# Optimization experiments

Hardware: AMD Instinct MI355X
Metric: run time of the kernel (lower is better)

## Reference

```python
import jax, jax.numpy as jnp
import numpy as np
import math

B, T, E, H = 2, 2048, 1024, 16
HD = E // H


def layernorm(x, g, b, eps=1e-5):
    mu = jnp.mean(x, axis=-1, keepdims=True)
    var = jnp.var(x, axis=-1, keepdims=True)
    return (x - mu) * jax.lax.rsqrt(var + eps) * g + b


def new_gelu(x):
    c = math.sqrt(2.0 / math.pi)
    return 0.5 * x * (1.0 + jnp.tanh(c * (x + 0.044715 * x ** 3)))


def setup_inputs() -> dict:
    key = jax.random.key(0)
    ks = jax.random.split(key, 6)
    s = 0.02
    return {
        "x": jax.random.normal(ks[0], (B, T, E), jnp.float32),
        "ln1_g": jnp.ones((E,), jnp.float32),
        "ln1_b": jnp.zeros((E,), jnp.float32),
        "w_attn": jax.random.normal(ks[1], (E, 3 * E), jnp.float32) * s,
        "b_attn": jnp.zeros((3 * E,), jnp.float32),
        "w_proj": jax.random.normal(ks[2], (E, E), jnp.float32) * s,
        "b_proj": jnp.zeros((E,), jnp.float32),
        "ln2_g": jnp.ones((E,), jnp.float32),
        "ln2_b": jnp.zeros((E,), jnp.float32),
        "w_fc": jax.random.normal(ks[3], (E, 4 * E), jnp.float32) * s,
        "b_fc": jnp.zeros((4 * E,), jnp.float32),
        "w_fc2": jax.random.normal(ks[4], (4 * E, E), jnp.float32) * s,
        "b_fc2": jnp.zeros((E,), jnp.float32),
    }


def reference(x, ln1_g, ln1_b, w_attn, b_attn, w_proj, b_proj,
              ln2_g, ln2_b, w_fc, b_fc, w_fc2, b_fc2):
    # --- attention branch (pre-norm) ---
    h = layernorm(x, ln1_g, ln1_b)
    qkv = h @ w_attn + b_attn                      # [B,T,3E]
    q, k, v = jnp.split(qkv, 3, axis=-1)
    # [B,T,E] -> [B,H,T,HD]
    q = q.reshape(B, T, H, HD).transpose(0, 2, 1, 3)
    k = k.reshape(B, T, H, HD).transpose(0, 2, 1, 3)
    v = v.reshape(B, T, H, HD).transpose(0, 2, 1, 3)
    att = jnp.einsum('bhqd,bhkd->bhqk', q, k) * (1.0 / math.sqrt(HD))
    causal = jnp.tril(jnp.ones((T, T), bool))       # [T,T]
    att = jnp.where(causal, att, -jnp.inf)
    att = jax.nn.softmax(att, axis=-1)
    y = jnp.einsum('bhqk,bhkd->bhqd', att, v)       # [B,H,T,HD]
    y = y.transpose(0, 2, 1, 3).reshape(B, T, E)
    y = y @ w_proj + b_proj
    x = x + y
    # --- MLP branch (pre-norm) ---
    h = layernorm(x, ln2_g, ln2_b)
    h = new_gelu(h @ w_fc + b_fc)
    h = h @ w_fc2 + b_fc2
    return x + h
```

## Files before the change

kernel.cpp:

```cpp
#include <hip/hip_runtime.h>

typedef unsigned short u16;
typedef unsigned int   u32;
typedef short bf16x8 __attribute__((ext_vector_type(8)));
typedef float f32x4  __attribute__((ext_vector_type(4)));

__device__ __forceinline__ float bf_lo(u32 u){ return __uint_as_float(u << 16); }
__device__ __forceinline__ float bf_hi(u32 u){ return __uint_as_float(u & 0xffff0000u); }
__device__ __forceinline__ u16 bf16r(float f){
  u32 u = __float_as_uint(f);
  u += 0x7fffu + ((u >> 16) & 1u);
  return (u16)(u >> 16);
}
__device__ __forceinline__ u32 pack2(float a, float b){
  return (u32)bf16r(a) | ((u32)bf16r(b) << 16);
}
__device__ __forceinline__ u32 pk_trunc(float a, float b){
  return (__float_as_uint(a) >> 16) | (__float_as_uint(b) & 0xffff0000u);
}
__device__ __forceinline__ float gelu_f(float x){
  float t = 0.7978845608028654f * (x + 0.044715f * x * x * x);
  t = fminf(fmaxf(t, -12.f), 12.f);
  float e = __expf(2.f * t);
  float th = (e - 1.f) / (e + 1.f);
  return 0.5f * x * (1.f + th);
}
__device__ __forceinline__ void glds16(const void* g, void* l) {
  __builtin_amdgcn_global_load_lds(
      (const __attribute__((address_space(1))) void*)g,
      (__attribute__((address_space(3))) void*)l, 16, 0, 0);
}

#define QSCALE 0.1803368801111204f

__device__ __forceinline__ void wt_body(const float* __restrict__ W,
                                        u16* __restrict__ Wt, int K, int N,
                                        int kx, int nx) {
  __shared__ float t[32][33];
  int k0 = kx * 32, n0 = nx * 32;
  int tx = threadIdx.x & 31, ty = threadIdx.x >> 5;
  #pragma unroll
  for (int i = 0; i < 32; i += 8)
    t[ty + i][tx] = W[(size_t)(k0 + ty + i) * N + n0 + tx];
  __syncthreads();
  #pragma unroll
  for (int i = 0; i < 32; i += 8)
    Wt[(size_t)(n0 + ty + i) * K + k0 + tx] = bf16r(t[tx][ty + i]);
}

__device__ __forceinline__ void ln_body(const float* __restrict__ x,
                                        const float* __restrict__ g,
                                        const float* __restrict__ bta,
                                        u16* __restrict__ out, int row) {
  int tid = threadIdx.x;
  const float4 xv = ((const float4*)(x + (size_t)row * 1024))[tid];
  float s = xv.x + xv.y + xv.z + xv.w;
  float q = xv.x*xv.x + xv.y*xv.y + xv.z*xv.z + xv.w*xv.w;
  #pragma unroll
  for (int off = 32; off > 0; off >>= 1) {
    s += __shfl_down(s, off);
    q += __shfl_down(q, off);
  }
  __shared__ float ss[4], sq[4];
  if ((tid & 63) == 0) { ss[tid >> 6] = s; sq[tid >> 6] = q; }
  __syncthreads();
  s = ss[0] + ss[1] + ss[2] + ss[3];
  q = sq[0] + sq[1] + sq[2] + sq[3];
  float mu = s * (1.f/1024.f);
  float rs = rsqrtf(q * (1.f/1024.f) - mu*mu + 1e-5f);
  const float4 gv = ((const float4*)g)[tid];
  const float4 bv = ((const float4*)bta)[tid];
  uint2 o;
  o.x = pack2((xv.x-mu)*rs*gv.x + bv.x, (xv.y-mu)*rs*gv.y + bv.y);
  o.y = pack2((xv.z-mu)*rs*gv.z + bv.z, (xv.w-mu)*rs*gv.w + bv.w);
  ((uint2*)(out + (size_t)row * 1024))[tid] = o;
}

__global__ __launch_bounds__(256) void prep_k(
    const float* __restrict__ w_attn, const float* __restrict__ w_proj,
    const float* __restrict__ w_fc,   const float* __restrict__ w_fc2,
    u16* __restrict__ wt_attn, u16* __restrict__ wt_proj,
    u16* __restrict__ wt_fc,   u16* __restrict__ wt_fc2,
    const float* __restrict__ x, const float* __restrict__ g,
    const float* __restrict__ b, u16* __restrict__ h1)
{
  int i = blockIdx.x;
  if (i < 3072)       wt_body(w_attn, wt_attn, 1024, 3072, i & 31, i >> 5);
  else if (i < 4096)  { int j = i - 3072; wt_body(w_proj, wt_proj, 1024, 1024, j & 31, j >> 5); }
  else if (i < 8192)  { int j = i - 4096; wt_body(w_fc,   wt_fc,   1024, 4096, j & 31, j >> 5); }
  else if (i < 12288) { int j = i - 8192; wt_body(w_fc2,  wt_fc2,  4096, 1024, j & 127, j >> 7); }
  else                ln_body(x, g, b, h1, i - 12288);
}

__global__ __launch_bounds__(256) void vt_k(const u16* __restrict__ qkv,
                                            u16* __restrict__ Vt) {
  __shared__ u16 tl[32][33];
  int t0 = blockIdx.x * 32;
  int bh = blockIdx.y >> 1, d0 = (blockIdx.y & 1) * 32;
  int bb = bh >> 4, h = bh & 15;
  int tx = threadIdx.x & 31, ty = threadIdx.x >> 5;
  #pragma unroll
  for (int i = 0; i < 32; i += 8)
    tl[ty + i][tx] = qkv[(size_t)(bb*2048 + t0 + ty + i)*3072 + 2048 + h*64 + d0 + tx];
  __syncthreads();
  #pragma unroll
  for (int i = 0; i < 32; i += 8)
    Vt[((size_t)bh*64 + d0 + ty + i)*2048 + t0 + tx] = tl[tx][ty + i];
}

__global__ __launch_bounds__(256) void ln_k(const float* __restrict__ x,
                                            const float* __restrict__ g,
                                            const float* __restrict__ bta,
                                            u16* __restrict__ out) {
  ln_body(x, g, bta, out, blockIdx.x);
}

template<int MODE, int MI, int LB>
__global__ __launch_bounds__(256, LB) void gemm_k(
    const u16* __restrict__ A, const u16* __restrict__ Bt,
    const float* __restrict__ bias, const float* __restrict__ resid,
    void* __restrict__ out, int M, int N, int K, int lda)
{
  constexpr int TM = MI * 32;
  __shared__ u16 Al[TM * 64];
  __shared__ u16 Bl[128 * 64];
  const int tid = threadIdx.x;
  const int by = blockIdx.y;
  const int sp = (MODE == 5) ? (by >> 3) : 0;
  const int n0 = (MODE == 5) ? ((by & 7) * 128) : (by * 128);
  const size_t koff = (size_t)sp * K;
  const int m0 = blockIdx.x * TM;
  const int wave = tid >> 6, lane = tid & 63;
  const int wm = (wave >> 1) * (MI * 16), wn = (wave & 1) * 64;
  const int l15 = lane & 15, quad = lane >> 4;
  const int sr = lane >> 3, cs = lane & 7;
  f32x4 acc[MI][4];
  const f32x4 zero = {0.f, 0.f, 0.f, 0.f};
  #pragma unroll
  for (int i = 0; i < MI; ++i)
    #pragma unroll
    for (int j = 0; j < 4; ++j)
      acc[i][j] = zero;
  for (int k0 = 0; k0 < K; k0 += 64) {
    __syncthreads();
    #pragma unroll
    for (int it = 0; it < MI; ++it) {
      int r = it*32 + wave*8 + sr;
      int c = cs ^ (r & 7);
      glds16(&A[(size_t)(m0 + r) * lda + koff + k0 + c*8], &Al[(it*32 + wave*8) * 64]);
    }
    #pragma unroll
    for (int it = 0; it < 4; ++it) {
      int r = it*32 + wave*8 + sr;
      int c = cs ^ (r & 7);
      glds16(&Bt[(size_t)(n0 + r) * lda + koff + k0 + c*8], &Bl[(it*32 + wave*8) * 64]);
    }
    __syncthreads();
    #pragma unroll
    for (int kk = 0; kk < 2; ++kk) {
      bf16x8 af[MI], bfr[4];
      #pragma unroll
      for (int i = 0; i < MI; ++i) {
        int R = wm + i*16 + l15;
        af[i] = *(const bf16x8*)&Al[R*64 + ((kk*4 + quad) ^ (R & 7)) * 8];
      }
      #pragma unroll
      for (int j = 0; j < 4; ++j) {
        int R = wn + j*16 + l15;
        bfr[j] = *(const bf16x8*)&Bl[R*64 + ((kk*4 + quad) ^ (R & 7)) * 8];
      }
      #pragma unroll
      for (int i = 0; i < MI; ++i)
        #pragma unroll
        for (int j = 0; j < 4; ++j)
          acc[i][j] = __builtin_amdgcn_mfma_f32_16x16x32_bf16(af[i], bfr[j], acc[i][j], 0, 0, 0);
    }
  }
  #pragma unroll
  for (int i = 0; i < MI; ++i) {
    #pragma unroll
    for (int j = 0; j < 4; ++j) {
      int col = n0 + wn + j*16 + l15;
      float bv = (MODE == 5) ? 0.f : bias[col];
      float sc = (MODE == 4 && col < 1024) ? QSCALE : 1.0f;
      #pragma unroll
      for (int r = 0; r < 4; ++r) {
        int row = m0 + wm + i*16 + quad*4 + r;
        size_t idx = (size_t)row * N + col;
        float v = acc[i][j][r] + bv;
        if constexpr (MODE == 0)      ((u16*)out)[idx] = bf16r(v);
        else if constexpr (MODE == 1) ((float*)out)[idx] = v + resid[idx];
        else if constexpr (MODE == 2) ((u16*)out)[idx] = bf16r(gelu_f(v));
        else if constexpr (MODE == 4) ((u16*)out)[idx] = bf16r(v * sc);
        else if constexpr (MODE == 5) ((u16*)out)[(size_t)sp*M*N + idx] = bf16r(v);
        else                          ((float*)out)[idx] = v + resid[idx];
      }
    }
  }
}

__global__ __launch_bounds__(256) void cmb_k(const u16* __restrict__ p,
                                             const float* __restrict__ bias,
                                             const float* __restrict__ x2,
                                             float* __restrict__ out) {
  int row = blockIdx.x, t = threadIdx.x;
  size_t i = (size_t)row * 1024 + t*4;
  uint2 a = *(const uint2*)&p[i];
  uint2 b = *(const uint2*)&p[4194304 + i];
  float4 xv = ((const float4*)x2)[i >> 2];
  float4 bv = ((const float4*)bias)[t];
  float4 o;
  o.x = bf_lo(a.x) + bf_lo(b.x) + bv.x + xv.x;
  o.y = bf_hi(a.x) + bf_hi(b.x) + bv.y + xv.y;
  o.z = bf_lo(a.y) + bf_lo(b.y) + bv.z + xv.z;
  o.w = bf_hi(a.y) + bf_hi(b.y) + bv.w + xv.w;
  ((float4*)out)[i >> 2] = o;
}

__global__ __launch_bounds__(256, 4) void attn_k(const u16* __restrict__ qkv,
                                                 const u16* __restrict__ Vt,
                                                 u16* __restrict__ y) {
  __shared__ u16 Kl[64*64];
  __shared__ u16 Vl[64*64];
  __shared__ u16 Pw[4*16*72];
  const int tid = threadIdx.x;
  const int bh = blockIdx.x & 31, bb = bh >> 4, h = bh & 15;
  const int qt = 31 - (int)(blockIdx.x >> 5);
  const int w = tid >> 6, lane = tid & 63;
  const int l15 = lane & 15, quad = lane >> 4;
  const int sr = lane >> 3, cs = lane & 7;
  u16* Pme = Pw + w * (16*72);
  const int w16l = w*16 + l15;
  const int dquad = quad*4;

  const u16* qp = qkv + ((size_t)(bb*2048 + qt*64 + w16l))*3072 + h*64 + quad*8;
  const bf16x8 aq0 = *(const bf16x8*)qp;
  const bf16x8 aq1 = *(const bf16x8*)(qp + 32);

  f32x4 o[4];
  const f32x4 zero = {0.f,0.f,0.f,0.f};
  #pragma unroll
  for (int dt = 0; dt < 4; ++dt) o[dt] = zero;
  float l = 0.f;

  const u16* kbase = qkv + (size_t)bb*2048*3072 + 1024 + h*64;
  const u16* vbase = Vt + (size_t)bh*64*2048;

  for (int kt = 0; kt <= qt; ++kt) {
    __syncthreads();
    #pragma unroll
    for (int it = 0; it < 2; ++it) {
      int r = it*32 + w*8 + sr;
      int c = cs ^ (r & 7);
      glds16(kbase + (size_t)(kt*64 + r)*3072 + c*8, &Kl[(it*32 + w*8) * 64]);
      glds16(vbase + (size_t)r*2048 + kt*64 + c*8,   &Vl[(it*32 + w*8) * 64]);
    }
    __syncthreads();
    bf16x8 ak[4][2], av[4][2];
    #pragma unroll
    for (int nt = 0; nt < 4; ++nt) {
      int R = nt*16 + l15;
      #pragma unroll
      for (int kk = 0; kk < 2; ++kk) {
        ak[nt][kk] = *(const bf16x8*)&Kl[R*64 + ((kk*4 + quad) ^ (R & 7)) * 8];
        av[nt][kk] = *(const bf16x8*)&Vl[R*64 + ((kk*4 + quad) ^ (R & 7)) * 8];
      }
    }
    f32x4 sv[4];
    #pragma unroll
    for (int nt = 0; nt < 4; ++nt) {
      f32x4 s = zero;
      s = __builtin_amdgcn_mfma_f32_16x16x32_bf16(ak[nt][0], aq0, s, 0, 0, 0);
      s = __builtin_amdgcn_mfma_f32_16x16x32_bf16(ak[nt][1], aq1, s, 0, 0, 0);
      sv[nt] = s;
    }
    if (kt == qt) {
      #pragma unroll
      for (int nt = 0; nt < 4; ++nt)
        #pragma unroll
        for (int r = 0; r < 4; ++r)
          if (nt*16 + dquad + r > w16l) sv[nt][r] = -1e30f;
    }
    float pv[4][4];
    #pragma unroll
    for (int nt = 0; nt < 4; ++nt)
      #pragma unroll
      for (int r = 0; r < 4; ++r)
        pv[nt][r] = exp2f(sv[nt][r]);
    l += ((pv[0][0]+pv[0][1])+(pv[0][2]+pv[0][3]))
       + ((pv[1][0]+pv[1][1])+(pv[1][2]+pv[1][3]))
       + ((pv[2][0]+pv[2][1])+(pv[2][2]+pv[2][3]))
       + ((pv[3][0]+pv[3][1])+(pv[3][2]+pv[3][3]));
    #pragma unroll
    for (int nt = 0; nt < 4; ++nt) {
      uint2 pr;
      pr.x = pk_trunc(pv[nt][0], pv[nt][1]);
      pr.y = pk_trunc(pv[nt][2], pv[nt][3]);
      *(uint2*)&Pme[l15*72 + nt*16 + dquad] = pr;
    }
    const bf16x8 bp0 = *(const bf16x8*)&Pme[l15*72 + quad*8];
    const bf16x8 bp1 = *(const bf16x8*)&Pme[l15*72 + 32 + quad*8];
    #pragma unroll
    for (int dt = 0; dt < 4; ++dt) {
      o[dt] = __builtin_amdgcn_mfma_f32_16x16x32_bf16(av[dt][0], bp0, o[dt], 0, 0, 0);
      o[dt] = __builtin_amdgcn_mfma_f32_16x16x32_bf16(av[dt][1], bp1, o[dt], 0, 0, 0);
    }
  }
  float lt = l;
  lt += __shfl_xor(lt, 16);
  lt += __shfl_xor(lt, 32);
  float inv = 1.f / lt;
  u16* yp = y + ((size_t)(bb*2048 + qt*64 + w16l))*1024 + h*64;
  #pragma unroll
  for (int dt = 0; dt < 4; ++dt) {
    uint2 pk;
    pk.x = pack2(o[dt][0]*inv, o[dt][1]*inv);
    pk.y = pack2(o[dt][2]*inv, o[dt][3]*inv);
    *(uint2*)(yp + dt*16 + dquad) = pk;
  }
}

extern "C" void kernel_launch(void* const* d_in, const int* in_sizes, int n_in,
                              void* d_out, int out_size, void* d_ws, size_t ws_size,
                              hipStream_t stream) {
  const float* x      = (const float*)d_in[0];
  const float* ln1_g  = (const float*)d_in[1];
  const float* ln1_b  = (const float*)d_in[2];
  const float* w_attn = (const float*)d_in[3];
  const float* b_attn = (const float*)d_in[4];
  const float* w_proj = (const float*)d_in[5];
  const float* b_proj = (const float*)d_in[6];
  const float* ln2_g  = (const float*)d_in[7];
  const float* ln2_b  = (const float*)d_in[8];
  const float* w_fc   = (const float*)d_in[9];
  const float* b_fc   = (const float*)d_in[10];
  const float* w_fc2  = (const float*)d_in[11];
  const float* b_fc2  = (const float*)d_in[12];

  char* ws = (char*)d_ws;
  u16*   wt_attn = (u16*)(ws);
  u16*   wt_proj = (u16*)(ws + 6291456);
  u16*   wt_fc   = (u16*)(ws + 8388608);
  u16*   wt_fc2  = (u16*)(ws + 16777216);
  u16*   h1      = (u16*)(ws + 25165824);
  u16*   qkvb    = (u16*)(ws + 33554432);
  u16*   yb      = (u16*)(ws + 58720256);
  float* x2      = (float*)(ws + 67108864);
  u16*   h2  = h1;
  u16*   vtb = h1;
  u16*   act = qkvb;
  u16*   pk2 = (u16*)(ws);

  prep_k<<<dim3(16384), 256, 0, stream>>>(w_attn, w_proj, w_fc, w_fc2,
                                          wt_attn, wt_proj, wt_fc, wt_fc2,
                                          x, ln1_g, ln1_b, h1);
  gemm_k<4,4,3><<<dim3(32, 24), 256, 0, stream>>>(h1, wt_attn, b_attn, nullptr,
                                                  (void*)qkvb, 4096, 3072, 1024, 1024);
  vt_k<<<dim3(64, 64), 256, 0, stream>>>(qkvb, vtb);
  attn_k<<<dim3(1024), 256, 0, stream>>>(qkvb, vtb, yb);
  gemm_k<1,2,3><<<dim3(64, 8), 256, 0, stream>>>(yb, wt_proj, b_proj, x,
                                                 (void*)x2, 4096, 1024, 1024, 1024);
  ln_k<<<4096, 256, 0, stream>>>(x2, ln2_g, ln2_b, h2);
  gemm_k<2,4,3><<<dim3(32, 32), 256, 0, stream>>>(h2, wt_fc, b_fc, nullptr,
                                                  (void*)act, 4096, 4096, 1024, 1024);
  gemm_k<5,2,3><<<dim3(64, 16), 256, 0, stream>>>(act, wt_fc2, b_fc2, nullptr,
                                                  (void*)pk2, 4096, 1024, 2048, 4096);
  cmb_k<<<4096, 256, 0, stream>>>(pk2, b_fc2, x2, (float*)d_out);
}
```

Baseline: 318.4 us.

## Split attention KV range across two blocks and fuse split-K reduction via atomics

Attention now launches twice as many blocks, each covering half of the causal key tiles. The two halves are merged through a global-memory handshake: the first block to finish stores a bf16 partial output and its row sums, and the second adds them in before normalising. The FC2 split-K GEMM uses the same first-writer/second-reducer scheme, which removes the separate combine kernel and its extra pass over memory. The aim is better load balance and occupancy for attention and one fewer launch, at the cost of memset launches, spin-waits that depend on both blocks being resident, and bf16 rounding of the partials.

```diff
diff --git a/kernel.cpp b/kernel.cpp
--- a/kernel.cpp
+++ b/kernel.cpp
@@ -119,15 +119,16 @@
 __global__ __launch_bounds__(256, LB) void gemm_k(
     const u16* __restrict__ A, const u16* __restrict__ Bt,
     const float* __restrict__ bias, const float* __restrict__ resid,
-    void* __restrict__ out, int M, int N, int K, int lda)
+    void* __restrict__ out, int M, int N, int K, int lda,
+    u16* __restrict__ part, int* __restrict__ tick, int* __restrict__ done)
 {
   constexpr int TM = MI * 32;
   __shared__ u16 Al[TM * 64];
   __shared__ u16 Bl[128 * 64];
   const int tid = threadIdx.x;
   const int by = blockIdx.y;
-  const int sp = (MODE == 5) ? (by >> 3) : 0;
-  const int n0 = (MODE == 5) ? ((by & 7) * 128) : (by * 128);
+  const int sp = (MODE == 6) ? (by >> 3) : 0;
+  const int n0 = (MODE == 6) ? ((by & 7) * 128) : (by * 128);
   const size_t koff = (size_t)sp * K;
   const int m0 = blockIdx.x * TM;
   const int wave = tid >> 6, lane = tid & 63;
@@ -176,12 +177,66 @@
           acc[i][j] = __builtin_amdgcn_mfma_f32_16x16x32_bf16(af[i], bfr[j], acc[i][j], 0, 0, 0);
     }
   }
+
+  if constexpr (MODE == 6) {
+    const int tile = blockIdx.x * 8 + (by & 7);
+    u16* blob = part + (size_t)tile * 8192 + tid * 32;
+    __shared__ int who;
+    if (tid == 0) who = atomicAdd(&tick[tile], 1);
+    __syncthreads();
+    if (who == 0) {
+      u32 pk[16]; int n = 0;
+      #pragma unroll
+      for (int i = 0; i < MI; ++i)
+        #pragma unroll
+        for (int j = 0; j < 4; ++j) {
+          pk[n++] = pack2(acc[i][j][0], acc[i][j][1]);
+          pk[n++] = pack2(acc[i][j][2], acc[i][j][3]);
+        }
+      #pragma unroll
+      for (int u = 0; u < 4; ++u)
+        ((uint4*)blob)[u] = ((uint4*)pk)[u];
+      __threadfence();
+      if (tid == 0) atomicExch(&done[tile], 1);
+    } else {
+      if (tid == 0) { while (atomicAdd(&done[tile], 0) == 0) {} }
+      __syncthreads();
+      __threadfence();
+      u32 pk[16];
+      #pragma unroll
+      for (int u = 0; u < 4; ++u)
+        ((uint4*)pk)[u] = ((const uint4*)blob)[u];
+      int n = 0;
+      #pragma unroll
+      for (int i = 0; i < MI; ++i)
+        #pragma unroll
+        for (int j = 0; j < 4; ++j) {
+          acc[i][j][0] += bf_lo(pk[n]);   acc[i][j][1] += bf_hi(pk[n]); ++n;
+          acc[i][j][2] += bf_lo(pk[n]);   acc[i][j][3] += bf_hi(pk[n]); ++n;
+        }
+      #pragma unroll
+      for (int i = 0; i < MI; ++i)
+        #pragma unroll
+        for (int j = 0; j < 4; ++j) {
+          int col = n0 + wn + j*16 + l15;
+          float bv = bias[col];
+          #pragma unroll
+          for (int r = 0; r < 4; ++r) {
+            int row = m0 + wm + i*16 + quad*4 + r;
+            size_t idx = (size_t)row * N + col;
+            ((float*)out)[idx] = acc[i][j][r] + bv + resid[idx];
+          }
+        }
+    }
+    return;
+  }
+
   #pragma unroll
   for (int i = 0; i < MI; ++i) {
     #pragma unroll
     for (int j = 0; j < 4; ++j) {
       int col = n0 + wn + j*16 + l15;
-      float bv = (MODE == 5) ? 0.f : bias[col];
+      float bv = bias[col];
       float sc = (MODE == 4 && col < 1024) ? QSCALE : 1.0f;
       #pragma unroll
       for (int r = 0; r < 4; ++r) {
@@ -192,40 +247,32 @@
         else if constexpr (MODE == 1) ((float*)out)[idx] = v + resid[idx];
         else if constexpr (MODE == 2) ((u16*)out)[idx] = bf16r(gelu_f(v));
         else if constexpr (MODE == 4) ((u16*)out)[idx] = bf16r(v * sc);
-        else if constexpr (MODE == 5) ((u16*)out)[(size_t)sp*M*N + idx] = bf16r(v);
         else                          ((float*)out)[idx] = v + resid[idx];
       }
     }
   }
 }
 
-__global__ __launch_bounds__(256) void cmb_k(const u16* __restrict__ p,
-                                             const float* __restrict__ bias,
-                                             const float* __restrict__ x2,
-                                             float* __restrict__ out) {
-  int row = blockIdx.x, t = threadIdx.x;
-  size_t i = (size_t)row * 1024 + t*4;
-  uint2 a = *(const uint2*)&p[i];
-  uint2 b = *(const uint2*)&p[4194304 + i];
-  float4 xv = ((const float4*)x2)[i >> 2];
-  float4 bv = ((const float4*)bias)[t];
-  float4 o;
-  o.x = bf_lo(a.x) + bf_lo(b.x) + bv.x + xv.x;
-  o.y = bf_hi(a.x) + bf_hi(b.x) + bv.y + xv.y;
-  o.z = bf_lo(a.y) + bf_lo(b.y) + bv.z + xv.z;
-  o.w = bf_hi(a.y) + bf_hi(b.y) + bv.w + xv.w;
-  ((float4*)out)[i >> 2] = o;
-}
-
 __global__ __launch_bounds__(256, 4) void attn_k(const u16* __restrict__ qkv,
                                                  const u16* __restrict__ Vt,
-                                                 u16* __restrict__ y) {
+                                                 u16* __restrict__ y,
+                                                 int* __restrict__ atick,
+                                                 int* __restrict__ adone,
+                                                 float* __restrict__ al,
+                                                 u16* __restrict__ ao) {
   __shared__ u16 Kl[64*64];
   __shared__ u16 Vl[64*64];
   __shared__ u16 Pw[4*16*72];
   const int tid = threadIdx.x;
-  const int bh = blockIdx.x & 31, bb = bh >> 4, h = bh & 15;
-  const int qt = 31 - (int)(blockIdx.x >> 5);
+  const int bid = blockIdx.x;
+  const int qt = 31 - (bid >> 6);
+  const int bh = (bid >> 1) & 31;
+  const int half = bid & 1;
+  const int bb = bh >> 4, h = bh & 15;
+  const int ntiles = qt + 1;
+  const int h0 = (ntiles + 1) >> 1;
+  const int k0t = half ? h0 : 0;
+  const int k1t = half ? ntiles : h0;
   const int w = tid >> 6, lane = tid & 63;
   const int l15 = lane & 15, quad = lane >> 4;
   const int sr = lane >> 3, cs = lane & 7;
@@ -246,7 +293,7 @@
   const u16* kbase = qkv + (size_t)bb*2048*3072 + 1024 + h*64;
   const u16* vbase = Vt + (size_t)bh*64*2048;
 
-  for (int kt = 0; kt <= qt; ++kt) {
+  for (int kt = k0t; kt < k1t; ++kt) {
     __syncthreads();
     #pragma unroll
     for (int it = 0; it < 2; ++it) {
@@ -305,6 +352,40 @@
       o[dt] = __builtin_amdgcn_mfma_f32_16x16x32_bf16(av[dt][0], bp0, o[dt], 0, 0, 0);
       o[dt] = __builtin_amdgcn_mfma_f32_16x16x32_bf16(av[dt][1], bp1, o[dt], 0, 0, 0);
     }
+  }
+
+  const int id = bh*32 + qt;
+  u16* oblob = ao + (size_t)id * 4096 + tid * 16;
+  __shared__ int who;
+  if (tid == 0) who = atomicAdd(&atick[id], 1);
+  __syncthreads();
+  if (who == 0) {
+    u32 pk[8];
+    #pragma unroll
+    for (int dt = 0; dt < 4; ++dt) {
+      pk[dt*2+0] = pack2(o[dt][0], o[dt][1]);
+      pk[dt*2+1] = pack2(o[dt][2], o[dt][3]);
+    }
+    ((uint4*)oblob)[0] = ((uint4*)pk)[0];
+    ((uint4*)oblob)[1] = ((uint4*)pk)[1];
+    al[id*256 + tid] = l;
+    __threadfence();
+    if (tid == 0) atomicExch(&adone[id], 1);
+    return;
+  }
+  if (tid == 0) { while (atomicAdd(&adone[id], 0) == 0) {} }
+  __syncthreads();
+  __threadfence();
+  {
+    u32 pk[8];
+    ((uint4*)pk)[0] = ((const uint4*)oblob)[0];
+    ((uint4*)pk)[1] = ((const uint4*)oblob)[1];
+    #pragma unroll
+    for (int dt = 0; dt < 4; ++dt) {
+      o[dt][0] += bf_lo(pk[dt*2+0]);  o[dt][1] += bf_hi(pk[dt*2+0]);
+      o[dt][2] += bf_lo(pk[dt*2+1]);  o[dt][3] += bf_hi(pk[dt*2+1]);
+    }
+    l += al[id*256 + tid];
   }
   float lt = l;
   lt += __shfl_xor(lt, 16);
@@ -349,21 +430,28 @@
   u16*   h2  = h1;
   u16*   vtb = h1;
   u16*   act = qkvb;
-  u16*   pk2 = (u16*)(ws);
+  u16*   fc2_part = (u16*)(ws);
+  int*   fc2_tick = (int*)(ws + 25165824);
+  int*   fc2_done = (int*)(ws + 25165824 + 2048);
+  int*   at_tick = (int*)(ws + 67108864);
+  int*   at_done = (int*)(ws + 67108864 + 4096);
+  float* at_l    = (float*)(ws + 67108864 + 16384);
+  u16*   at_o    = (u16*)(ws + 67108864 + 16384 + 1048576);
 
   prep_k<<<dim3(16384), 256, 0, stream>>>(w_attn, w_proj, w_fc, w_fc2,
                                           wt_attn, wt_proj, wt_fc, wt_fc2,
                                           x, ln1_g, ln1_b, h1);
   gemm_k<4,4,3><<<dim3(32, 24), 256, 0, stream>>>(h1, wt_attn, b_attn, nullptr,
-                                                  (void*)qkvb, 4096, 3072, 1024, 1024);
+      (void*)qkvb, 4096, 3072, 1024, 1024, nullptr, nullptr, nullptr);
   vt_k<<<dim3(64, 64), 256, 0, stream>>>(qkvb, vtb);
-  attn_k<<<dim3(1024), 256, 0, stream>>>(qkvb, vtb, yb);
+  hipMemsetAsync(at_tick, 0, 8192, stream);
+  attn_k<<<dim3(2048), 256, 0, stream>>>(qkvb, vtb, yb, at_tick, at_done, at_l, at_o);
   gemm_k<1,2,3><<<dim3(64, 8), 256, 0, stream>>>(yb, wt_proj, b_proj, x,
-                                                 (void*)x2, 4096, 1024, 1024, 1024);
+      (void*)x2, 4096, 1024, 1024, 1024, nullptr, nullptr, nullptr);
   ln_k<<<4096, 256, 0, stream>>>(x2, ln2_g, ln2_b, h2);
   gemm_k<2,4,3><<<dim3(32, 32), 256, 0, stream>>>(h2, wt_fc, b_fc, nullptr,
-                                                  (void*)act, 4096, 4096, 1024, 1024);
-  gemm_k<5,2,3><<<dim3(64, 16), 256, 0, stream>>>(act, wt_fc2, b_fc2, nullptr,
-                                                  (void*)pk2, 4096, 1024, 2048, 4096);
-  cmb_k<<<4096, 256, 0, stream>>>(pk2, b_fc2, x2, (float*)d_out);
-}
+      (void*)act, 4096, 4096, 1024, 1024, nullptr, nullptr, nullptr);
+  hipMemsetAsync(fc2_tick, 0, 4096, stream);
+  gemm_k<6,2,3><<<dim3(64, 16), 256, 0, stream>>>(act, wt_fc2, b_fc2, x2,
+      d_out, 4096, 1024, 2048, 4096, fc2_part, fc2_tick, fc2_done);
+}
```

Measured after the change: 714.5 us. +124.4%, slower.

## Split attention key tiles across warp pairs with 32-row query tiles

Applied to the files above, without the earlier changes.

Each attention block now handles 32 query rows instead of 64. Its four warps are arranged as two query halves times two key halves, and each warp processes 32 of the 64 keys in a tile. Partial O and row-sum accumulators from the two key halves are combined through shared memory at the end. This doubles the grid to 2048 blocks and raises the occupancy hint to 6, aiming for better load balance across the causal triangle and more parallelism. In exchange, each K/V tile is loaded per 32 query rows instead of 64, which doubles K/V traffic, and the final reduction adds an extra shared-memory pass and barrier.

```diff
diff --git a/kernel.cpp b/kernel.cpp
--- a/kernel.cpp
+++ b/kernel.cpp
@@ -217,23 +217,24 @@
   ((float4*)out)[i >> 2] = o;
 }
 
-__global__ __launch_bounds__(256, 4) void attn_k(const u16* __restrict__ qkv,
+__global__ __launch_bounds__(256, 6) void attn_k(const u16* __restrict__ qkv,
                                                  const u16* __restrict__ Vt,
                                                  u16* __restrict__ y) {
-  __shared__ u16 Kl[64*64];
-  __shared__ u16 Vl[64*64];
-  __shared__ u16 Pw[4*16*72];
+  __shared__ __align__(16) u16 Kl[64*64];
+  __shared__ __align__(16) u16 Vl[64*64];
+  __shared__ u16 Pw[4*16*40];
   const int tid = threadIdx.x;
   const int bh = blockIdx.x & 31, bb = bh >> 4, h = bh & 15;
-  const int qt = 31 - (int)(blockIdx.x >> 5);
+  const int qt = 63 - (int)(blockIdx.x >> 5);
   const int w = tid >> 6, lane = tid & 63;
+  const int qh = w & 1, kh = w >> 1;
   const int l15 = lane & 15, quad = lane >> 4;
   const int sr = lane >> 3, cs = lane & 7;
-  u16* Pme = Pw + w * (16*72);
-  const int w16l = w*16 + l15;
+  u16* Pme = Pw + w * (16*40);
   const int dquad = quad*4;
-
-  const u16* qp = qkv + ((size_t)(bb*2048 + qt*64 + w16l))*3072 + h*64 + quad*8;
+  const int qrow = qt*32 + qh*16 + l15;
+
+  const u16* qp = qkv + ((size_t)(bb*2048 + qrow))*3072 + h*64 + quad*8;
   const bf16x8 aq0 = *(const bf16x8*)qp;
   const bf16x8 aq1 = *(const bf16x8*)(qp + 32);
 
@@ -245,8 +246,9 @@
 
   const u16* kbase = qkv + (size_t)bb*2048*3072 + 1024 + h*64;
   const u16* vbase = Vt + (size_t)bh*64*2048;
-
-  for (int kt = 0; kt <= qt; ++kt) {
+  const int ntk = qt/2 + 1;
+
+  for (int kt = 0; kt < ntk; ++kt) {
     __syncthreads();
     #pragma unroll
     for (int it = 0; it < 2; ++it) {
@@ -256,67 +258,81 @@
       glds16(vbase + (size_t)r*2048 + kt*64 + c*8,   &Vl[(it*32 + w*8) * 64]);
     }
     __syncthreads();
-    bf16x8 ak[4][2], av[4][2];
-    #pragma unroll
-    for (int nt = 0; nt < 4; ++nt) {
-      int R = nt*16 + l15;
-      #pragma unroll
-      for (int kk = 0; kk < 2; ++kk) {
-        ak[nt][kk] = *(const bf16x8*)&Kl[R*64 + ((kk*4 + quad) ^ (R & 7)) * 8];
-        av[nt][kk] = *(const bf16x8*)&Vl[R*64 + ((kk*4 + quad) ^ (R & 7)) * 8];
-      }
-    }
-    f32x4 sv[4];
-    #pragma unroll
-    for (int nt = 0; nt < 4; ++nt) {
-      f32x4 s = zero;
-      s = __builtin_amdgcn_mfma_f32_16x16x32_bf16(ak[nt][0], aq0, s, 0, 0, 0);
-      s = __builtin_amdgcn_mfma_f32_16x16x32_bf16(ak[nt][1], aq1, s, 0, 0, 0);
-      sv[nt] = s;
-    }
-    if (kt == qt) {
-      #pragma unroll
-      for (int nt = 0; nt < 4; ++nt)
+    f32x4 sv[2];
+    #pragma unroll
+    for (int s = 0; s < 2; ++s) {
+      int R = (kh*2 + s)*16 + l15;
+      const bf16x8 ak0 = *(const bf16x8*)&Kl[R*64 + ((0 + quad) ^ (R & 7)) * 8];
+      const bf16x8 ak1 = *(const bf16x8*)&Kl[R*64 + ((4 + quad) ^ (R & 7)) * 8];
+      f32x4 sacc = zero;
+      sacc = __builtin_amdgcn_mfma_f32_16x16x32_bf16(ak0, aq0, sacc, 0, 0, 0);
+      sacc = __builtin_amdgcn_mfma_f32_16x16x32_bf16(ak1, aq1, sacc, 0, 0, 0);
+      sv[s] = sacc;
+    }
+    if (kt == ntk - 1) {
+      #pragma unroll
+      for (int s = 0; s < 2; ++s)
         #pragma unroll
-        for (int r = 0; r < 4; ++r)
-          if (nt*16 + dquad + r > w16l) sv[nt][r] = -1e30f;
-    }
-    float pv[4][4];
-    #pragma unroll
-    for (int nt = 0; nt < 4; ++nt)
+        for (int r = 0; r < 4; ++r) {
+          int key = kt*64 + (kh*2 + s)*16 + dquad + r;
+          if (key > qrow) sv[s][r] = -1e30f;
+        }
+    }
+    float pv[2][4];
+    #pragma unroll
+    for (int s = 0; s < 2; ++s)
       #pragma unroll
       for (int r = 0; r < 4; ++r)
-        pv[nt][r] = exp2f(sv[nt][r]);
+        pv[s][r] = exp2f(sv[s][r]);
     l += ((pv[0][0]+pv[0][1])+(pv[0][2]+pv[0][3]))
-       + ((pv[1][0]+pv[1][1])+(pv[1][2]+pv[1][3]))
-       + ((pv[2][0]+pv[2][1])+(pv[2][2]+pv[2][3]))
-       + ((pv[3][0]+pv[3][1])+(pv[3][2]+pv[3][3]));
-    #pragma unroll
-    for (int nt = 0; nt < 4; ++nt) {
+       + ((pv[1][0]+pv[1][1])+(pv[1][2]+pv[1][3]));
+    #pragma unroll
+    for (int s = 0; s < 2; ++s) {
       uint2 pr;
-      pr.x = pk_trunc(pv[nt][0], pv[nt][1]);
-      pr.y = pk_trunc(pv[nt][2], pv[nt][3]);
-      *(uint2*)&Pme[l15*72 + nt*16 + dquad] = pr;
-    }
-    const bf16x8 bp0 = *(const bf16x8*)&Pme[l15*72 + quad*8];
-    const bf16x8 bp1 = *(const bf16x8*)&Pme[l15*72 + 32 + quad*8];
+      pr.x = pk_trunc(pv[s][0], pv[s][1]);
+      pr.y = pk_trunc(pv[s][2], pv[s][3]);
+      *(uint2*)&Pme[l15*40 + s*16 + dquad] = pr;
+    }
+    const bf16x8 bp = *(const bf16x8*)&Pme[l15*40 + quad*8];
     #pragma unroll
     for (int dt = 0; dt < 4; ++dt) {
-      o[dt] = __builtin_amdgcn_mfma_f32_16x16x32_bf16(av[dt][0], bp0, o[dt], 0, 0, 0);
-      o[dt] = __builtin_amdgcn_mfma_f32_16x16x32_bf16(av[dt][1], bp1, o[dt], 0, 0, 0);
-    }
-  }
-  float lt = l;
-  lt += __shfl_xor(lt, 16);
-  lt += __shfl_xor(lt, 32);
-  float inv = 1.f / lt;
-  u16* yp = y + ((size_t)(bb*2048 + qt*64 + w16l))*1024 + h*64;
-  #pragma unroll
-  for (int dt = 0; dt < 4; ++dt) {
-    uint2 pk;
-    pk.x = pack2(o[dt][0]*inv, o[dt][1]*inv);
-    pk.y = pack2(o[dt][2]*inv, o[dt][3]*inv);
-    *(uint2*)(yp + dt*16 + dquad) = pk;
+      int R = dt*16 + l15;
+      const bf16x8 av = *(const bf16x8*)&Vl[R*64 + (((kh*4) + quad) ^ (R & 7)) * 8];
+      o[dt] = __builtin_amdgcn_mfma_f32_16x16x32_bf16(av, bp, o[dt], 0, 0, 0);
+    }
+  }
+
+  __syncthreads();
+  float* obuf = (float*)Kl;
+  float* lbuf = (float*)Vl;
+  if (kh == 1) {
+    #pragma unroll
+    for (int dt = 0; dt < 4; ++dt)
+      #pragma unroll
+      for (int r = 0; r < 4; ++r)
+        obuf[(dt*4 + r)*128 + qh*64 + lane] = o[dt][r];
+    lbuf[qh*64 + lane] = l;
+  }
+  __syncthreads();
+  if (kh == 0) {
+    #pragma unroll
+    for (int dt = 0; dt < 4; ++dt)
+      #pragma unroll
+      for (int r = 0; r < 4; ++r)
+        o[dt][r] += obuf[(dt*4 + r)*128 + qh*64 + lane];
+    l += lbuf[qh*64 + lane];
+    float lt = l;
+    lt += __shfl_xor(lt, 16);
+    lt += __shfl_xor(lt, 32);
+    float inv = 1.f / lt;
+    u16* yp = y + ((size_t)(bb*2048 + qrow))*1024 + h*64;
+    #pragma unroll
+    for (int dt = 0; dt < 4; ++dt) {
+      uint2 pk;
+      pk.x = pack2(o[dt][0]*inv, o[dt][1]*inv);
+      pk.y = pack2(o[dt][2]*inv, o[dt][3]*inv);
+      *(uint2*)(yp + dt*16 + dquad) = pk;
+    }
   }
 }
 
@@ -357,7 +373,7 @@
   gemm_k<4,4,3><<<dim3(32, 24), 256, 0, stream>>>(h1, wt_attn, b_attn, nullptr,
                                                   (void*)qkvb, 4096, 3072, 1024, 1024);
   vt_k<<<dim3(64, 64), 256, 0, stream>>>(qkvb, vtb);
-  attn_k<<<dim3(1024), 256, 0, stream>>>(qkvb, vtb, yb);
+  attn_k<<<dim3(2048), 256, 0, stream>>>(qkvb, vtb, yb);
   gemm_k<1,2,3><<<dim3(64, 8), 256, 0, stream>>>(yb, wt_proj, b_proj, x,
                                                  (void*)x2, 4096, 1024, 1024, 1024);
   ln_k<<<4096, 256, 0, stream>>>(x2, ln2_g, ln2_b, h2);
```

Result: slower. 327.4 us (+2.8%).
